# Kernel optimization log

Measured on AMD Instinct MI355X. Metric: run time of the kernel, lower is better.

The kernel has to match this reference:

```python
import jax, jax.numpy as jnp
import numpy as np

N_NODES = 50000
N_EDGES = 800000


def gcn_conv(x, edge_index, W, b):
    """PyG GCNConv: add self-loops, symmetric deg^{-1/2} normalization,
    dense transform, scatter-add aggregation."""
    n = x.shape[0]
    src, dst = edge_index[0], edge_index[1]
    # add self-loops
    loop = jnp.arange(n, dtype=src.dtype)
    src = jnp.concatenate([src, loop])
    dst = jnp.concatenate([dst, loop])
    # degree on destination nodes (includes self-loops -> deg >= 1)
    deg = jax.ops.segment_sum(jnp.ones_like(dst, dtype=x.dtype), dst, num_segments=n)
    dinv = jax.lax.rsqrt(deg)
    norm = dinv[src] * dinv[dst]  # [E+N]
    h = x @ W                     # [N, F_out] dense GEMM
    msg = h[src] * norm[:, None]  # gather + scale, [E+N, F_out]
    out = jax.ops.segment_sum(msg, dst, num_segments=n)  # scatter-add
    return out + b


def setup_inputs() -> dict:
    key = jax.random.key(0)
    ks = jax.random.split(key, 8)
    x = jax.random.normal(ks[0], (N_NODES, 100), dtype=jnp.float32)
    edge_index = jax.random.randint(ks[1], (2, N_EDGES), 0, N_NODES, dtype=jnp.int64)
    W1 = jax.random.normal(ks[2], (100, 256), dtype=jnp.float32) * 0.1
    b1 = jnp.zeros((256,), dtype=jnp.float32)
    W2 = jax.random.normal(ks[3], (256, 128), dtype=jnp.float32) * 0.06
    b2 = jnp.zeros((128,), dtype=jnp.float32)
    Wfc = jax.random.normal(ks[4], (128, 1), dtype=jnp.float32) * 0.09
    bfc = jnp.zeros((1,), dtype=jnp.float32)
    return {"x": x, "edge_index": edge_index, "W1": W1, "b1": b1,
            "W2": W2, "b2": b2, "Wfc": Wfc, "bfc": bfc}


def reference(x, edge_index, W1, b1, W2, b2, Wfc, bfc):
    # eval mode: F.dropout with training=False is identity
    h = jax.nn.relu(gcn_conv(x, edge_index, W1, b1))
    h = jax.nn.relu(gcn_conv(h, edge_index, W2, b2))
    return h @ Wfc + bfc  # [N, 1]
```

## Files before the change

kernel.cpp:

```cpp
#include <hip/hip_runtime.h>
#include <hip/hip_bf16.h>


#define F0 100
#define F1 256
#define F2 128


__global__ void zero_i32(int* p, int n) {
    int i = blockIdx.x * blockDim.x + threadIdx.x;
    if (i < n) p[i] = 0;
}

__global__ void deg_count_i(const int* __restrict__ dst, int* deg, int e) {
    int i = blockIdx.x * blockDim.x + threadIdx.x;
    if (i < e) atomicAdd(deg + dst[i], 1);
}

__global__ __launch_bounds__(256) void scan1(const int* __restrict__ deg,
                                             int* __restrict__ excl,
                                             int* __restrict__ bsum,
                                             float* __restrict__ dinv, int n) {
    __shared__ int wsum[4];
    int i = blockIdx.x * 256 + threadIdx.x;
    int lane = threadIdx.x & 63, wid = threadIdx.x >> 6;
    int v = (i < n) ? deg[i] : 0;
    if (i < n) dinv[i] = rsqrtf((float)(v + 1));
    int s = v;
#pragma unroll
    for (int off = 1; off < 64; off <<= 1) {
        int t = __shfl_up(s, off, 64);
        if (lane >= off) s += t;
    }
    if (lane == 63) wsum[wid] = s;
    __syncthreads();
    int add = 0;
    for (int w = 0; w < wid; w++) add += wsum[w];
    if (i < n) excl[i] = add + s - v;
    if (threadIdx.x == 255) bsum[blockIdx.x] = add + s;
}

__global__ __launch_bounds__(256) void scan2(int* __restrict__ bsum, int nb,
                                             int* __restrict__ rowptr, int n) {
    __shared__ int wsum[4];
    int lane = threadIdx.x & 63, wid = threadIdx.x >> 6;
    int v = (threadIdx.x < nb) ? bsum[threadIdx.x] : 0;
    int s = v;
#pragma unroll
    for (int off = 1; off < 64; off <<= 1) {
        int t = __shfl_up(s, off, 64);
        if (lane >= off) s += t;
    }
    if (lane == 63) wsum[wid] = s;
    __syncthreads();
    int add = 0;
    for (int w = 0; w < wid; w++) add += wsum[w];
    if (threadIdx.x < nb) bsum[threadIdx.x] = add + s - v;
    if (threadIdx.x == 255) rowptr[n] = add + s;
}

__global__ void scan3(const int* __restrict__ excl, const int* __restrict__ bsum,
                      int* __restrict__ rowptr, int* __restrict__ cursor, int n) {
    int i = blockIdx.x * 256 + threadIdx.x;
    if (i < n) {
        int r = excl[i] + bsum[blockIdx.x];
        rowptr[i] = r;
        cursor[i] = r;
    }
}

__global__ void csr_fill(const int* __restrict__ src, const int* __restrict__ dst,
                         int* cursor, int* __restrict__ csr, int e) {
    int i = blockIdx.x * blockDim.x + threadIdx.x;
    if (i < e) {
        int pos = atomicAdd(cursor + dst[i], 1);
        csr[pos] = src[i];
    }
}

__global__ void scale_x(const float4* __restrict__ x4,
                        const float* __restrict__ dinv,
                        float4* __restrict__ xs4, int n25) {
    int i = blockIdx.x * blockDim.x + threadIdx.x;
    if (i < n25) {
        float d = dinv[i / 25];
        float4 v = x4[i];
        v.x *= d; v.y *= d; v.z *= d; v.w *= d;
        xs4[i] = v;
    }
}


__global__ __launch_bounds__(256) void pull_f100(
        const float* __restrict__ xs, const int* __restrict__ rowptr,
        const int* __restrict__ csr, const float* __restrict__ dinv,
        float* __restrict__ agg, int n) {
    int wave = threadIdx.x >> 6, lane = threadIdx.x & 63;
    int v = blockIdx.x * 4 + wave;
    if (v >= n) return;
    int beg = rowptr[v], end = rowptr[v + 1];
    float dv = dinv[v];
    int half = lane >> 5, q = lane & 31;
    bool act = q < 25;
    float4 acc = {0.f, 0.f, 0.f, 0.f};
    if (half == 0 && act) acc = ((const float4*)(xs + (size_t)v * F0))[q];

    for (int base = beg; base < end; base += 64) {
        int cnt = min(64, end - base);
        int sidx = (lane < cnt) ? csr[base + lane] : 0;
        int npf = cnt >> 1;
        int p = 0;
        for (; p + 4 <= npf; p += 4) {
            int s0 = __shfl(sidx, 2 * p + half, 64);
            int s1 = __shfl(sidx, 2 * p + 2 + half, 64);
            int s2 = __shfl(sidx, 2 * p + 4 + half, 64);
            int s3 = __shfl(sidx, 2 * p + 6 + half, 64);
            if (act) {
                float4 r0 = ((const float4*)(xs + (size_t)s0 * F0))[q];
                float4 r1 = ((const float4*)(xs + (size_t)s1 * F0))[q];
                float4 r2 = ((const float4*)(xs + (size_t)s2 * F0))[q];
                float4 r3 = ((const float4*)(xs + (size_t)s3 * F0))[q];
                acc.x += (r0.x + r1.x) + (r2.x + r3.x);
                acc.y += (r0.y + r1.y) + (r2.y + r3.y);
                acc.z += (r0.z + r1.z) + (r2.z + r3.z);
                acc.w += (r0.w + r1.w) + (r2.w + r3.w);
            }
        }
        for (; p < npf; p++) {
            int s0 = __shfl(sidx, 2 * p + half, 64);
            if (act) {
                float4 r0 = ((const float4*)(xs + (size_t)s0 * F0))[q];
                acc.x += r0.x; acc.y += r0.y; acc.z += r0.z; acc.w += r0.w;
            }
        }
        if (cnt & 1) {
            int sl = __shfl(sidx, cnt - 1, 64);
            if (half == 0 && act) {
                float4 r = ((const float4*)(xs + (size_t)sl * F0))[q];
                acc.x += r.x; acc.y += r.y; acc.z += r.z; acc.w += r.w;
            }
        }
    }
    float ox = __shfl_down(acc.x, 32, 64);
    float oy = __shfl_down(acc.y, 32, 64);
    float oz = __shfl_down(acc.z, 32, 64);
    float ow = __shfl_down(acc.w, 32, 64);
    if (half == 0 && act) {
        float4 r;
        r.x = dv * (acc.x + ox);
        r.y = dv * (acc.y + oy);
        r.z = dv * (acc.z + oz);
        r.w = dv * (acc.w + ow);
        ((float4*)(agg + (size_t)v * F0))[q] = r;
    }
}

__global__ __launch_bounds__(256) void pull_f128_fused(
        const float* __restrict__ h2s, const int* __restrict__ rowptr,
        const int* __restrict__ csr, const float* __restrict__ dinv,
        const float* __restrict__ b2, const float* __restrict__ Wfc,
        const float* __restrict__ bfc, float* __restrict__ out, int n) {
    int wave = threadIdx.x >> 6, lane = threadIdx.x & 63;
    int v = blockIdx.x * 4 + wave;
    if (v >= n) return;
    int beg = rowptr[v], end = rowptr[v + 1];
    float dv = dinv[v];
    int half = lane >> 5, q = lane & 31;
    float4 acc = {0.f, 0.f, 0.f, 0.f};
    if (half == 0) acc = ((const float4*)(h2s + (size_t)v * F2))[q];

    for (int base = beg; base < end; base += 64) {
        int cnt = min(64, end - base);
        int sidx = (lane < cnt) ? csr[base + lane] : 0;
        int npf = cnt >> 1;
        int p = 0;
        for (; p + 4 <= npf; p += 4) {
            int s0 = __shfl(sidx, 2 * p + half, 64);
            int s1 = __shfl(sidx, 2 * p + 2 + half, 64);
            int s2 = __shfl(sidx, 2 * p + 4 + half, 64);
            int s3 = __shfl(sidx, 2 * p + 6 + half, 64);
            float4 r0 = ((const float4*)(h2s + (size_t)s0 * F2))[q];
            float4 r1 = ((const float4*)(h2s + (size_t)s1 * F2))[q];
            float4 r2 = ((const float4*)(h2s + (size_t)s2 * F2))[q];
            float4 r3 = ((const float4*)(h2s + (size_t)s3 * F2))[q];
            acc.x += (r0.x + r1.x) + (r2.x + r3.x);
            acc.y += (r0.y + r1.y) + (r2.y + r3.y);
            acc.z += (r0.z + r1.z) + (r2.z + r3.z);
            acc.w += (r0.w + r1.w) + (r2.w + r3.w);
        }
        for (; p < npf; p++) {
            int s0 = __shfl(sidx, 2 * p + half, 64);
            float4 r0 = ((const float4*)(h2s + (size_t)s0 * F2))[q];
            acc.x += r0.x; acc.y += r0.y; acc.z += r0.z; acc.w += r0.w;
        }
        if (cnt & 1) {
            int sl = __shfl(sidx, cnt - 1, 64);
            if (half == 0) {
                float4 r = ((const float4*)(h2s + (size_t)sl * F2))[q];
                acc.x += r.x; acc.y += r.y; acc.z += r.z; acc.w += r.w;
            }
        }
    }
    float ox = __shfl_down(acc.x, 32, 64);
    float oy = __shfl_down(acc.y, 32, 64);
    float oz = __shfl_down(acc.z, 32, 64);
    float ow = __shfl_down(acc.w, 32, 64);
    if (half == 0) {
        float4 b2v = ((const float4*)b2)[q];
        float4 wv = ((const float4*)Wfc)[q];
        float t0 = dv * (acc.x + ox);
        float t1 = dv * (acc.y + oy);
        float t2 = dv * (acc.z + oz);
        float t3 = dv * (acc.w + ow);
        float part = fmaxf(t0 + b2v.x, 0.f) * wv.x + fmaxf(t1 + b2v.y, 0.f) * wv.y +
                     fmaxf(t2 + b2v.z, 0.f) * wv.z + fmaxf(t3 + b2v.w, 0.f) * wv.w;
        part += __shfl_down(part, 16, 64);
        part += __shfl_down(part, 8, 64);
        part += __shfl_down(part, 4, 64);
        part += __shfl_down(part, 2, 64);
        part += __shfl_down(part, 1, 64);
        if (lane == 0) out[v] = part + bfc[0];
    }
}


__global__ __launch_bounds__(256) void gemm1_tiled(
        const float* __restrict__ A, const float* __restrict__ W,
        const float* __restrict__ bias, float* __restrict__ C, int n) {
    __shared__ float As[20 * 128];
    __shared__ float Bs[20 * 128];
    int tid = threadIdx.x;
    int r0 = blockIdx.x * 128;
    int c0 = blockIdx.y * 128;
    int tc = tid & 15, tr = tid >> 4;
    float acc[8][8] = {};

    for (int k0 = 0; k0 < F0; k0 += 20) {
        if (k0) __syncthreads();
        for (int idx = tid; idx < 128 * 5; idx += 256) {
            int row = idx & 127, kq = idx >> 7;
            int gr = r0 + row;
            if (gr >= n) gr = n - 1;
            float4 v = *(const float4*)(A + (size_t)gr * F0 + k0 + 4 * kq);
            As[(4 * kq + 0) * 128 + row] = v.x;
            As[(4 * kq + 1) * 128 + row] = v.y;
            As[(4 * kq + 2) * 128 + row] = v.z;
            As[(4 * kq + 3) * 128 + row] = v.w;
        }
        for (int idx = tid; idx < 20 * 32; idx += 256) {
            int k = idx >> 5, cq = idx & 31;
            *(float4*)(Bs + k * 128 + 4 * cq) =
                *(const float4*)(W + (size_t)(k0 + k) * F1 + c0 + 4 * cq);
        }
        __syncthreads();
#pragma unroll 5
        for (int k = 0; k < 20; k++) {
            float4 a0 = *(const float4*)(As + k * 128 + 4 * tr);
            float4 a1 = *(const float4*)(As + k * 128 + 64 + 4 * tr);
            float4 b0 = *(const float4*)(Bs + k * 128 + 4 * tc);
            float4 b1 = *(const float4*)(Bs + k * 128 + 64 + 4 * tc);
            float av[8] = {a0.x, a0.y, a0.z, a0.w, a1.x, a1.y, a1.z, a1.w};
            float bv[8] = {b0.x, b0.y, b0.z, b0.w, b1.x, b1.y, b1.z, b1.w};
#pragma unroll
            for (int i = 0; i < 8; i++)
#pragma unroll
                for (int j = 0; j < 8; j++) acc[i][j] += av[i] * bv[j];
        }
    }
    float4 bb0 = *(const float4*)(bias + c0 + 4 * tc);
    float4 bb1 = *(const float4*)(bias + c0 + 64 + 4 * tc);
    float bv[8] = {bb0.x, bb0.y, bb0.z, bb0.w, bb1.x, bb1.y, bb1.z, bb1.w};
#pragma unroll
    for (int i = 0; i < 8; i++) {
        int row = (i < 4) ? (4 * tr + i) : (64 + 4 * tr + i - 4);
        int gr = r0 + row;
        if (gr < n) {
            float4 o0, o1;
            o0.x = fmaxf(acc[i][0] + bv[0], 0.f);
            o0.y = fmaxf(acc[i][1] + bv[1], 0.f);
            o0.z = fmaxf(acc[i][2] + bv[2], 0.f);
            o0.w = fmaxf(acc[i][3] + bv[3], 0.f);
            o1.x = fmaxf(acc[i][4] + bv[4], 0.f);
            o1.y = fmaxf(acc[i][5] + bv[5], 0.f);
            o1.z = fmaxf(acc[i][6] + bv[6], 0.f);
            o1.w = fmaxf(acc[i][7] + bv[7], 0.f);
            *(float4*)(C + (size_t)gr * F1 + c0 + 4 * tc) = o0;
            *(float4*)(C + (size_t)gr * F1 + c0 + 64 + 4 * tc) = o1;
        }
    }
}

__global__ __launch_bounds__(256) void gemm2_tiled(
        const float* __restrict__ A, const float* __restrict__ W,
        const float* __restrict__ dinv, float* __restrict__ C, int n) {
    __shared__ float As[32 * 128];
    __shared__ float Bs[32 * 128];
    int tid = threadIdx.x;
    int r0 = blockIdx.x * 128;
    int tc = tid & 15, tr = tid >> 4;
    float acc[8][8] = {};

    for (int k0 = 0; k0 < F1; k0 += 32) {
        if (k0) __syncthreads();
        for (int idx = tid; idx < 128 * 8; idx += 256) {
            int row = idx & 127, kq = idx >> 7;
            int gr = r0 + row;
            if (gr >= n) gr = n - 1;
            float4 v = *(const float4*)(A + (size_t)gr * F1 + k0 + 4 * kq);
            As[(4 * kq + 0) * 128 + row] = v.x;
            As[(4 * kq + 1) * 128 + row] = v.y;
            As[(4 * kq + 2) * 128 + row] = v.z;
            As[(4 * kq + 3) * 128 + row] = v.w;
        }
        for (int idx = tid; idx < 32 * 32; idx += 256) {
            int k = idx >> 5, cq = idx & 31;
            *(float4*)(Bs + k * 128 + 4 * cq) =
                *(const float4*)(W + (size_t)(k0 + k) * F2 + 4 * cq);
        }
        __syncthreads();
#pragma unroll 4
        for (int k = 0; k < 32; k++) {
            float4 a0 = *(const float4*)(As + k * 128 + 4 * tr);
            float4 a1 = *(const float4*)(As + k * 128 + 64 + 4 * tr);
            float4 b0 = *(const float4*)(Bs + k * 128 + 4 * tc);
            float4 b1 = *(const float4*)(Bs + k * 128 + 64 + 4 * tc);
            float av[8] = {a0.x, a0.y, a0.z, a0.w, a1.x, a1.y, a1.z, a1.w};
            float bv[8] = {b0.x, b0.y, b0.z, b0.w, b1.x, b1.y, b1.z, b1.w};
#pragma unroll
            for (int i = 0; i < 8; i++)
#pragma unroll
                for (int j = 0; j < 8; j++) acc[i][j] += av[i] * bv[j];
        }
    }
#pragma unroll
    for (int i = 0; i < 8; i++) {
        int row = (i < 4) ? (4 * tr + i) : (64 + 4 * tr + i - 4);
        int gr = r0 + row;
        if (gr < n) {
            float d = dinv[gr];
            float4 o0 = {acc[i][0] * d, acc[i][1] * d, acc[i][2] * d, acc[i][3] * d};
            float4 o1 = {acc[i][4] * d, acc[i][5] * d, acc[i][6] * d, acc[i][7] * d};
            *(float4*)(C + (size_t)gr * F2 + 4 * tc) = o0;
            *(float4*)(C + (size_t)gr * F2 + 64 + 4 * tc) = o1;
        }
    }
}


static inline size_t align16(size_t x) { return (x + 3) & ~(size_t)3; }

extern "C" void kernel_launch(void* const* d_in, const int* in_sizes, int n_in,
                              void* d_out, int out_size, void* d_ws, size_t ws_size,
                              hipStream_t stream) {
    const float* x   = (const float*)d_in[0];
    const int*   ei  = (const int*)d_in[1];
    const float* W1  = (const float*)d_in[2];
    const float* b1  = (const float*)d_in[3];
    const float* W2  = (const float*)d_in[4];
    const float* b2  = (const float*)d_in[5];
    const float* Wfc = (const float*)d_in[6];
    const float* bfc = (const float*)d_in[7];
    float* out = (float*)d_out;

    const int n = in_sizes[0] / F0;
    const int e = in_sizes[1] / 2;
    const int* src = ei;
    const int* dst = ei + e;

    char* wsb = (char*)d_ws;
    size_t off = 0;
    int* deg    = (int*)(wsb + 4 * off); off = align16(off + n);
    int* excl   = (int*)(wsb + 4 * off); off = align16(off + n);
    int* bsum   = (int*)(wsb + 4 * off); off = align16(off + 256);
    int* rowptr = (int*)(wsb + 4 * off); off = align16(off + n + 1);
    int* cursor = (int*)(wsb + 4 * off); off = align16(off + n);
    int* csr    = (int*)(wsb + 4 * off); off = align16(off + e);
    float* dinv = (float*)(wsb + 4 * off); off = align16(off + n);
    float* xs   = (float*)(wsb + 4 * off); off = align16(off + (size_t)n * F0);
    float* aggX = (float*)(wsb + 4 * off); off = align16(off + (size_t)n * F0);
    float* a1   = (float*)(wsb + 4 * off); off = align16(off + (size_t)n * F1);
    float* h2s  = (float*)(wsb + 4 * off); off = align16(off + (size_t)n * F2);

    const int B = 256;
    const int nb = (n + B - 1) / B;
    const int rblocks = (n + 127) / 128;

    zero_i32<<<nb, B, 0, stream>>>(deg, n);
    deg_count_i<<<(e + B - 1) / B, B, 0, stream>>>(dst, deg, e);
    scan1<<<nb, B, 0, stream>>>(deg, excl, bsum, dinv, n);
    scale_x<<<((n * 25) + B - 1) / B, B, 0, stream>>>(
        (const float4*)x, dinv, (float4*)xs, n * 25);
    scan2<<<1, B, 0, stream>>>(bsum, nb, rowptr, n);
    scan3<<<nb, B, 0, stream>>>(excl, bsum, rowptr, cursor, n);
    csr_fill<<<(e + B - 1) / B, B, 0, stream>>>(src, dst, cursor, csr, e);

    pull_f100<<<(n + 3) / 4, 256, 0, stream>>>(xs, rowptr, csr, dinv, aggX, n);
    gemm1_tiled<<<dim3(rblocks, F1 / 128), 256, 0, stream>>>(aggX, W1, b1, a1, n);

    gemm2_tiled<<<rblocks, 256, 0, stream>>>(a1, W2, dinv, h2s, n);
    pull_f128_fused<<<(n + 3) / 4, 256, 0, stream>>>(h2s, rowptr, csr, dinv,
                                                     b2, Wfc, bfc, out, n);
}
```

Before: 389.9 us.

## Split layer-2 features into 16-wide column chunks for cache-friendly gather

```diff
diff --git a/kernel.cpp b/kernel.cpp
--- a/kernel.cpp
+++ b/kernel.cpp
@@ -10,6 +10,11 @@
 __global__ void zero_i32(int* p, int n) {
     int i = blockIdx.x * blockDim.x + threadIdx.x;
     if (i < n) p[i] = 0;
+}
+
+__global__ void fill_f32(float* out, const float* __restrict__ bfc, int n) {
+    int i = blockIdx.x * blockDim.x + threadIdx.x;
+    if (i < n) out[i] = bfc[0];
 }
 
 __global__ void deg_count_i(const int* __restrict__ dst, int* deg, int e) {
@@ -155,72 +160,55 @@
     }
 }
 
-__global__ __launch_bounds__(256) void pull_f128_fused(
-        const float* __restrict__ h2s, const int* __restrict__ rowptr,
+__global__ __launch_bounds__(256) void pull_c16_fused(
+        const float* __restrict__ h2c, const int* __restrict__ rowptr,
         const int* __restrict__ csr, const float* __restrict__ dinv,
         const float* __restrict__ b2, const float* __restrict__ Wfc,
-        const float* __restrict__ bfc, float* __restrict__ out, int n) {
+        float* __restrict__ out, int n) {
+    int chunk = blockIdx.x & 7;
+    int nb = blockIdx.x >> 3;
     int wave = threadIdx.x >> 6, lane = threadIdx.x & 63;
-    int v = blockIdx.x * 4 + wave;
+    int v = nb * 4 + wave;
     if (v >= n) return;
     int beg = rowptr[v], end = rowptr[v + 1];
     float dv = dinv[v];
-    int half = lane >> 5, q = lane & 31;
+    int q = lane & 3;
+    int g = lane >> 2;
+    const float* __restrict__ tab = h2c + (size_t)chunk * n * 16;
+
     float4 acc = {0.f, 0.f, 0.f, 0.f};
-    if (half == 0) acc = ((const float4*)(h2s + (size_t)v * F2))[q];
+    if (g == 0) acc = ((const float4*)(tab + (size_t)v * 16))[q];
 
     for (int base = beg; base < end; base += 64) {
         int cnt = min(64, end - base);
-        int sidx = (lane < cnt) ? csr[base + lane] : 0;
-        int npf = cnt >> 1;
-        int p = 0;
-        for (; p + 4 <= npf; p += 4) {
-            int s0 = __shfl(sidx, 2 * p + half, 64);
-            int s1 = __shfl(sidx, 2 * p + 2 + half, 64);
-            int s2 = __shfl(sidx, 2 * p + 4 + half, 64);
-            int s3 = __shfl(sidx, 2 * p + 6 + half, 64);
-            float4 r0 = ((const float4*)(h2s + (size_t)s0 * F2))[q];
-            float4 r1 = ((const float4*)(h2s + (size_t)s1 * F2))[q];
-            float4 r2 = ((const float4*)(h2s + (size_t)s2 * F2))[q];
-            float4 r3 = ((const float4*)(h2s + (size_t)s3 * F2))[q];
-            acc.x += (r0.x + r1.x) + (r2.x + r3.x);
-            acc.y += (r0.y + r1.y) + (r2.y + r3.y);
-            acc.z += (r0.z + r1.z) + (r2.z + r3.z);
-            acc.w += (r0.w + r1.w) + (r2.w + r3.w);
-        }
-        for (; p < npf; p++) {
-            int s0 = __shfl(sidx, 2 * p + half, 64);
-            float4 r0 = ((const float4*)(h2s + (size_t)s0 * F2))[q];
-            acc.x += r0.x; acc.y += r0.y; acc.z += r0.z; acc.w += r0.w;
-        }
-        if (cnt & 1) {
-            int sl = __shfl(sidx, cnt - 1, 64);
-            if (half == 0) {
-                float4 r = ((const float4*)(h2s + (size_t)sl * F2))[q];
+        int sidx = (lane < cnt) ? __builtin_nontemporal_load(csr + base + lane) : 0;
+        int iters = (cnt + 15) >> 4;
+        for (int it = 0; it < iters; ++it) {
+            int e = (it << 4) + g;
+            int s = __shfl(sidx, e, 64);
+            if (e < cnt) {
+                float4 r = ((const float4*)(tab + (size_t)s * 16))[q];
                 acc.x += r.x; acc.y += r.y; acc.z += r.z; acc.w += r.w;
             }
         }
     }
-    float ox = __shfl_down(acc.x, 32, 64);
-    float oy = __shfl_down(acc.y, 32, 64);
-    float oz = __shfl_down(acc.z, 32, 64);
-    float ow = __shfl_down(acc.w, 32, 64);
-    if (half == 0) {
-        float4 b2v = ((const float4*)b2)[q];
-        float4 wv = ((const float4*)Wfc)[q];
-        float t0 = dv * (acc.x + ox);
-        float t1 = dv * (acc.y + oy);
-        float t2 = dv * (acc.z + oz);
-        float t3 = dv * (acc.w + ow);
-        float part = fmaxf(t0 + b2v.x, 0.f) * wv.x + fmaxf(t1 + b2v.y, 0.f) * wv.y +
-                     fmaxf(t2 + b2v.z, 0.f) * wv.z + fmaxf(t3 + b2v.w, 0.f) * wv.w;
-        part += __shfl_down(part, 16, 64);
-        part += __shfl_down(part, 8, 64);
-        part += __shfl_down(part, 4, 64);
-        part += __shfl_down(part, 2, 64);
-        part += __shfl_down(part, 1, 64);
-        if (lane == 0) out[v] = part + bfc[0];
-    }
+#pragma unroll
+    for (int off = 4; off < 64; off <<= 1) {
+        acc.x += __shfl_xor(acc.x, off, 64);
+        acc.y += __shfl_xor(acc.y, off, 64);
+        acc.z += __shfl_xor(acc.z, off, 64);
+        acc.w += __shfl_xor(acc.w, off, 64);
+    }
+    int c0 = chunk * 16 + 4 * q;
+    float4 bb = *(const float4*)(b2 + c0);
+    float4 ww = *(const float4*)(Wfc + c0);
+    float part = fmaxf(fmaf(dv, acc.x, bb.x), 0.f) * ww.x
+               + fmaxf(fmaf(dv, acc.y, bb.y), 0.f) * ww.y
+               + fmaxf(fmaf(dv, acc.z, bb.z), 0.f) * ww.z
+               + fmaxf(fmaf(dv, acc.w, bb.w), 0.f) * ww.w;
+    part += __shfl_xor(part, 1, 64);
+    part += __shfl_xor(part, 2, 64);
+    if (lane == 0) atomicAdd(out + v, part);
 }
 
 
@@ -332,6 +320,8 @@
                 for (int j = 0; j < 8; j++) acc[i][j] += av[i] * bv[j];
         }
     }
+    int ch = tc >> 2;
+    int of = (tc & 3) << 2;
 #pragma unroll
     for (int i = 0; i < 8; i++) {
         int row = (i < 4) ? (4 * tr + i) : (64 + 4 * tr + i - 4);
@@ -340,8 +330,8 @@
             float d = dinv[gr];
             float4 o0 = {acc[i][0] * d, acc[i][1] * d, acc[i][2] * d, acc[i][3] * d};
             float4 o1 = {acc[i][4] * d, acc[i][5] * d, acc[i][6] * d, acc[i][7] * d};
-            *(float4*)(C + (size_t)gr * F2 + 4 * tc) = o0;
-            *(float4*)(C + (size_t)gr * F2 + 64 + 4 * tc) = o1;
+            *(float4*)(C + ((size_t)ch * n + gr) * 16 + of) = o0;
+            *(float4*)(C + ((size_t)(ch + 4) * n + gr) * 16 + of) = o1;
         }
     }
 }
@@ -379,13 +369,14 @@
     float* xs   = (float*)(wsb + 4 * off); off = align16(off + (size_t)n * F0);
     float* aggX = (float*)(wsb + 4 * off); off = align16(off + (size_t)n * F0);
     float* a1   = (float*)(wsb + 4 * off); off = align16(off + (size_t)n * F1);
-    float* h2s  = (float*)(wsb + 4 * off); off = align16(off + (size_t)n * F2);
+    float* h2c  = (float*)(wsb + 4 * off); off = align16(off + (size_t)n * F2);
 
     const int B = 256;
     const int nb = (n + B - 1) / B;
     const int rblocks = (n + 127) / 128;
 
     zero_i32<<<nb, B, 0, stream>>>(deg, n);
+    fill_f32<<<nb, B, 0, stream>>>(out, bfc, n);
     deg_count_i<<<(e + B - 1) / B, B, 0, stream>>>(dst, deg, e);
     scan1<<<nb, B, 0, stream>>>(deg, excl, bsum, dinv, n);
     scale_x<<<((n * 25) + B - 1) / B, B, 0, stream>>>(
@@ -397,7 +388,7 @@
     pull_f100<<<(n + 3) / 4, 256, 0, stream>>>(xs, rowptr, csr, dinv, aggX, n);
     gemm1_tiled<<<dim3(rblocks, F1 / 128), 256, 0, stream>>>(aggX, W1, b1, a1, n);
 
-    gemm2_tiled<<<rblocks, 256, 0, stream>>>(a1, W2, dinv, h2s, n);
-    pull_f128_fused<<<(n + 3) / 4, 256, 0, stream>>>(h2s, rowptr, csr, dinv,
-                                                     b2, Wfc, bfc, out, n);
-}
+    gemm2_tiled<<<rblocks, 256, 0, stream>>>(a1, W2, dinv, h2c, n);
+    pull_c16_fused<<<8 * ((n + 3) / 4), 256, 0, stream>>>(
+        h2c, rowptr, csr, dinv, b2, Wfc, out, n);
+}
```

After: 465.1 us. 1.19x slower.
